# Kernel optimization log

Measured on AMD Instinct MI355X. Metric: run time of the kernel, lower is better.

## Reference

```python
import jax, jax.numpy as jnp
import numpy as np

B = 32
C = 768
NH = 12
HD = C // NH
P = 16
IMG = 224
G = IMG // P           # 14 patches per side
NP = G * G             # 196 patches
DEPTH = 12
PRUNE = [1, 1, 1, 1, 0.5, 0.5, 0.5, 0.5, 0.5, 0.5, 0.5, 0.5]
MOM = 0.5              # momentum for global class-attention update
TRADE = 0.5            # slow-fast tradeoff for placeholder token update
SCALE = HD ** -0.5
NCLS = 1000

def _ln(x, g, b, eps=1e-6):
    mu = jnp.mean(x, -1, keepdims=True)
    var = jnp.mean((x - mu) ** 2, -1, keepdims=True)
    return (x - mu) * jax.lax.rsqrt(var + eps) * g + b

def setup_inputs():
    key = jax.random.key(0)
    ks = iter(jax.random.split(key, 40))
    def rn(shape, s=0.02):
        return jax.random.normal(next(ks), shape, jnp.float32) * s
    return {
        'x_img': jax.random.normal(next(ks), (B, 3, IMG, IMG), jnp.float32),
        'cls_token': rn((1, 1, C)),
        'pos_embed': rn((1, NP + 1, C)),
        'patch_w': rn((3 * P * P, C)),
        'patch_b': rn((C,)),
        'ln1_g': jnp.ones((DEPTH, C), jnp.float32),
        'ln1_b': jnp.zeros((DEPTH, C), jnp.float32),
        'qk_w': rn((DEPTH, C, 2 * C)),
        'qk_b': rn((DEPTH, 2 * C)),
        'v_w': rn((DEPTH, C, C)),
        'v_b': rn((DEPTH, C)),
        'proj_w': rn((DEPTH, C, C)),
        'proj_b': rn((DEPTH, C)),
        'ln2_g': jnp.ones((DEPTH, C), jnp.float32),
        'ln2_b': jnp.zeros((DEPTH, C), jnp.float32),
        'fc1_w': rn((DEPTH, C, 4 * C)),
        'fc1_b': rn((DEPTH, 4 * C)),
        'fc2_w': rn((DEPTH, 4 * C, C)),
        'fc2_b': rn((DEPTH, C)),
        'norm_g': jnp.ones((C,), jnp.float32),
        'norm_b': jnp.zeros((C,), jnp.float32),
        'head_w': rn((C, NCLS)),
        'head_b': rn((NCLS,)),
    }

def reference(x_img, cls_token, pos_embed, patch_w, patch_b, ln1_g, ln1_b,
              qk_w, qk_b, v_w, v_b, proj_w, proj_b, ln2_g, ln2_b,
              fc1_w, fc1_b, fc2_w, fc2_b, norm_g, norm_b, head_w, head_b):
    Bq = x_img.shape[0]
    # PatchEmbed: Conv2d(k=P, stride=P) == flatten each patch as (c, ph, pw) then matmul
    patches = x_img.reshape(Bq, 3, G, P, G, P).transpose(0, 2, 4, 1, 3, 5)
    patches = patches.reshape(Bq, NP, 3 * P * P)
    x = patches @ patch_w + patch_b                                   # [B,196,C]
    x = jnp.concatenate([jnp.broadcast_to(cls_token, (Bq, 1, C)), x], 1)
    x = x + pos_embed                                                 # [B,197,C]

    def block(xt, i):
        # QKAttention + VAttention + proj residual, then MlpBlock residual.
        t = _ln(xt, ln1_g[i], ln1_b[i])
        Nt = t.shape[1]
        qk = (t @ qk_w[i] + qk_b[i]).reshape(Bq, Nt, 2, NH, HD)
        q = qk[:, :, 0].transpose(0, 2, 1, 3)                         # [B,H,Nt,hd]
        k = qk[:, :, 1].transpose(0, 2, 1, 3)
        attn = jax.nn.softmax(jnp.einsum('bhnd,bhmd->bhnm', q, k) * SCALE, -1)
        v = (t @ v_w[i] + v_b[i]).reshape(Bq, Nt, NH, HD).transpose(0, 2, 1, 3)
        o = jnp.einsum('bhnm,bhmd->bhnd', attn, v).transpose(0, 2, 1, 3).reshape(Bq, Nt, C)
        xt = xt + (o @ proj_w[i] + proj_b[i])
        h = _ln(xt, ln2_g[i], ln2_b[i])
        xt = xt + (jax.nn.gelu(h @ fc1_w[i] + fc1_b[i], approximate=False) @ fc2_w[i] + fc2_b[i])
        row = attn[:, :, 0, 1:].sum(1)   # cls-attention row, summed over heads
        return xt, row

    cls_attn = None
    for i in range(DEPTH):
        if PRUNE[i] == 1:
            x, row = block(x, i)
            cls_attn = row if cls_attn is None else (1 - MOM) * cls_attn + MOM * row
        else:
            N_ = int(NP * PRUNE[i])                        # informative token count
            idx = jnp.argsort(-cls_attn, axis=1)           # sort patches by score (easy_gather)
            xp = jnp.take_along_axis(x[:, 1:], idx[:, :, None], axis=1)
            cls_attn = jnp.take_along_axis(cls_attn, idx, axis=1)
            fast = xp[:, N_:]                              # placeholder (pruned) tokens
            score = cls_attn[:, N_:]
            rep = (fast * score[:, :, None]).sum(1, keepdims=True) \
                  / score.sum(1, keepdims=True)[:, :, None]  # representative token
            xs = jnp.concatenate([x[:, :1], xp[:, :N_], rep], 1)   # [B,N_+2,C]
            xs, row = block(xs, i)
            cls_attn = jnp.concatenate(
                [(1 - MOM) * cls_attn[:, :N_] + MOM * row[:, :N_], cls_attn[:, N_:]], 1)
            fast = fast + TRADE * (xs[:, -1:] - rep)       # fast update via rep residual
            x = jnp.concatenate([xs[:, :N_ + 1], fast], 1)  # back to [B,197,C]

    x = _ln(x, norm_g, norm_b)
    return x[:, 0] @ head_w + head_b                        # [B,1000]
```

## Files before the change

### kernel.cpp

```cpp
#include <hip/hip_runtime.h>
#include <hip/hip_bf16.h>
#include <stdint.h>

#define B_ 32
#define C_ 768
#define NH_ 12
#define HD_ 64
#define NP_ 196
#define NTOK 197
#define NKEEP 98
#define NCLS_ 1000
#define MPAD 6400
#define RS_ (3 * C_)

typedef __bf16 bf16x8 __attribute__((ext_vector_type(8)));
typedef float f32x4 __attribute__((ext_vector_type(4)));

__device__ __forceinline__ float blockReduceSum256(float v) {
    __shared__ float red[4];
    const int lane = threadIdx.x & 63, w = threadIdx.x >> 6;
#pragma unroll
    for (int off = 32; off; off >>= 1) v += __shfl_down(v, off);
    __syncthreads();
    if (lane == 0) red[w] = v;
    __syncthreads();
    return red[0] + red[1] + red[2] + red[3];
}

__device__ __forceinline__ void gload16(void* lds, const void* g) {
    __builtin_amdgcn_global_load_lds(
        (const __attribute__((address_space(1))) void*)g,
        (__attribute__((address_space(3))) void*)lds,
        16, 0, 0);
}

__global__ __launch_bounds__(256) void patchify_kernel(const float* __restrict__ img,
                                                       __hip_bfloat16* __restrict__ patches)
{
    const int bp = blockIdx.x;
    const int b = bp / NP_, p = bp % NP_;
    const int gy = p / 14, gx = p % 14;
    const int tid = threadIdx.x;
#pragma unroll
    for (int j = 0; j < 3; ++j) {
        const int e = tid + j * 256;
        const int c = e >> 8, rem = e & 255, py = rem >> 4, px = rem & 15;
        patches[(size_t)bp * C_ + e] = __float2bfloat16(
            img[(((size_t)b * 3 + c) * 224 + gy * 16 + py) * 224 + gx * 16 + px]);
    }
}

__global__ __launch_bounds__(256) void assemble_x_kernel(const float* __restrict__ pemb,
                                                         const float* __restrict__ cls_tok,
                                                         const float* __restrict__ pos,
                                                         float* __restrict__ x)
{
    const int b = blockIdx.x, t = blockIdx.y, tid = threadIdx.x;
#pragma unroll
    for (int j = 0; j < 3; ++j) {
        const int c = tid + j * 256;
        const float v = (t == 0) ? cls_tok[c] : pemb[((size_t)b * NP_ + (t - 1)) * C_ + c];
        x[((size_t)b * NTOK + t) * C_ + c] = v + pos[(size_t)t * C_ + c];
    }
}

__global__ __launch_bounds__(256) void ln_kernel(const float* __restrict__ x,
                                                 const float* __restrict__ g,
                                                 const float* __restrict__ b,
                                                 __hip_bfloat16* outB, float* outF,
                                                 long long inRowStride, int nRows)
{
    const int row = (blockIdx.x << 2) + (threadIdx.x >> 6);
    const int lane = threadIdx.x & 63;
    if (row >= nRows) return;
    const float* xr = x + (size_t)row * inRowStride;
    float4 v0 = *(const float4*)(xr + (lane << 2));
    float4 v1 = *(const float4*)(xr + 256 + (lane << 2));
    float4 v2 = *(const float4*)(xr + 512 + (lane << 2));
    float s = v0.x + v0.y + v0.z + v0.w + v1.x + v1.y + v1.z + v1.w
            + v2.x + v2.y + v2.z + v2.w;
#pragma unroll
    for (int off = 1; off < 64; off <<= 1) s += __shfl_xor(s, off);
    const float mu = s * (1.f / C_);
    float q = 0.f;
    {
        float d;
        d = v0.x - mu; q += d * d; d = v0.y - mu; q += d * d;
        d = v0.z - mu; q += d * d; d = v0.w - mu; q += d * d;
        d = v1.x - mu; q += d * d; d = v1.y - mu; q += d * d;
        d = v1.z - mu; q += d * d; d = v1.w - mu; q += d * d;
        d = v2.x - mu; q += d * d; d = v2.y - mu; q += d * d;
        d = v2.z - mu; q += d * d; d = v2.w - mu; q += d * d;
    }
#pragma unroll
    for (int off = 1; off < 64; off <<= 1) q += __shfl_xor(q, off);
    const float rs = rsqrtf(q * (1.f / C_) + 1e-6f);
    const float4 vv[3] = {v0, v1, v2};
#pragma unroll
    for (int j = 0; j < 3; ++j) {
        const int cbase = (j << 8) + (lane << 2);
        const float4 gv = *(const float4*)(g + cbase);
        const float4 bv = *(const float4*)(b + cbase);
        float o0 = (vv[j].x - mu) * rs * gv.x + bv.x;
        float o1 = (vv[j].y - mu) * rs * gv.y + bv.y;
        float o2 = (vv[j].z - mu) * rs * gv.z + bv.z;
        float o3 = (vv[j].w - mu) * rs * gv.w + bv.w;
        if (outB) {
            union { unsigned short us[4]; uint2 u; } pk;
            __hip_bfloat16 h;
            h = __float2bfloat16(o0); pk.us[0] = *(unsigned short*)&h;
            h = __float2bfloat16(o1); pk.us[1] = *(unsigned short*)&h;
            h = __float2bfloat16(o2); pk.us[2] = *(unsigned short*)&h;
            h = __float2bfloat16(o3); pk.us[3] = *(unsigned short*)&h;
            *(uint2*)((unsigned short*)outB + (size_t)row * C_ + cbase) = pk.u;
        }
        if (outF) {
            float4 o; o.x = o0; o.y = o1; o.z = o2; o.w = o3;
            *(float4*)(outF + (size_t)row * C_ + cbase) = o;
        }
    }
}

__global__ __launch_bounds__(256) void transpose_bf16_kernel(const float* __restrict__ W,
                                                             __hip_bfloat16* __restrict__ Wt,
                                                             int K, int N,
                                                             long long outLstride, long long outOff)
{
    __shared__ float tile[32][33];
    const size_t loffIn = (size_t)blockIdx.z * K * N;
    const size_t loffOut = (size_t)blockIdx.z * outLstride + outOff;
    const int k0 = blockIdx.y << 5, n0 = blockIdx.x << 5;
    const int tid = threadIdx.x;
#pragma unroll
    for (int e = tid; e < 1024; e += 256) {
        const int r = e >> 5, c = e & 31;
        tile[r][c] = W[loffIn + (size_t)(k0 + r) * N + n0 + c];
    }
    __syncthreads();
#pragma unroll
    for (int e = tid; e < 1024; e += 256) {
        const int r = e >> 5, c = e & 31;
        Wt[loffOut + (size_t)(n0 + r) * K + k0 + c] = __float2bfloat16(tile[c][r]);
    }
}

__global__ __launch_bounds__(256) void concat_bias_kernel(const float* __restrict__ qk_b,
                                                          const float* __restrict__ v_b,
                                                          float* __restrict__ out)
{
    const int i = blockIdx.x * 256 + threadIdx.x;
    if (i < 12 * RS_) {
        const int l = i / RS_, c = i % RS_;
        out[i] = (c < 2 * C_) ? qk_b[l * 2 * C_ + c] : v_b[l * C_ + (c - 2 * C_)];
    }
}

template<int GELU, int OMODE>
__global__ __launch_bounds__(256) void gemm_bf16_kernel(const __hip_bfloat16* __restrict__ A,
                                                        const __hip_bfloat16* __restrict__ Bt,
                                                        const float* __restrict__ bias,
                                                        const float* __restrict__ res,
                                                        float* __restrict__ outF,
                                                        __hip_bfloat16* __restrict__ outB,
                                                        int K, int N)
{
    __shared__ __align__(16) unsigned short sAB[2][128 * 64];
    unsigned short* sA = sAB[0];
    unsigned short* sB = sAB[1];
    const int tid = threadIdx.x;
    const int wv = tid >> 6, ln = tid & 63;

    const int nwg = gridDim.x * gridDim.y;
    int lid = blockIdx.y * gridDim.x + blockIdx.x;
    {
        const int q = nwg >> 3, r = nwg & 7;
        const int xcd = lid & 7, lq = lid >> 3;
        lid = (xcd < r ? xcd * (q + 1) : r * (q + 1) + (xcd - r) * q) + lq;
    }
    const int bn = (lid % gridDim.x) << 7;
    const int bm = (lid / gridDim.x) << 7;

    const int wr = wv >> 1, wc = wv & 1;
    const int ln15 = ln & 15, lhi = ln >> 4;

    const int srow = tid >> 3;
    const int gc = (tid & 7) ^ ((tid >> 3) & 7);
    const __hip_bfloat16* gA = A + (size_t)(bm + srow) * K + (gc << 3);
    const __hip_bfloat16* gB = Bt + (size_t)(bn + srow) * K + (gc << 3);
    unsigned short* lA = sA + (wv << 9);
    unsigned short* lB = sB + (wv << 9);

    f32x4 acc[4][4] = {};
    const int swk = ln15 & 7;
    for (int k0 = 0; k0 < K; k0 += 64) {
#pragma unroll
        for (int i = 0; i < 4; ++i) {
            gload16(lA + (i << 11), gA + (size_t)(i << 5) * K + k0);
            gload16(lB + (i << 11), gB + (size_t)(i << 5) * K + k0);
        }
        __syncthreads();
#pragma unroll
        for (int kk = 0; kk < 2; ++kk) {
            const int ch = ((kk << 2) + lhi) ^ swk;
            bf16x8 a[4], b[4];
#pragma unroll
            for (int m = 0; m < 4; ++m)
                a[m] = *(const bf16x8*)(sA + (((wr << 6) + (m << 4) + ln15) << 6) + (ch << 3));
#pragma unroll
            for (int n = 0; n < 4; ++n)
                b[n] = *(const bf16x8*)(sB + (((wc << 6) + (n << 4) + ln15) << 6) + (ch << 3));
#pragma unroll
            for (int m = 0; m < 4; ++m)
#pragma unroll
                for (int n = 0; n < 4; ++n)
                    acc[m][n] = __builtin_amdgcn_mfma_f32_16x16x32_bf16(a[m], b[n], acc[m][n], 0, 0, 0);
        }
        __syncthreads();
    }

    if (OMODE == 0) {
        unsigned short* sOut = sAB[0];
#pragma unroll
        for (int n = 0; n < 4; ++n) {
            const int col = (wc << 6) + (n << 4) + ln15;
            const float bv = bias[bn + col];
#pragma unroll
            for (int m = 0; m < 4; ++m) {
                const int row0 = (wr << 6) + (m << 4) + (lhi << 2);
#pragma unroll
                for (int r = 0; r < 4; ++r) {
                    float x = acc[m][n][r] + bv;
                    if (GELU) x = 0.5f * x * (1.f + erff(x * 0.70710678118654752f));
                    const __hip_bfloat16 hb = __float2bfloat16(x);
                    sOut[(row0 + r) * 128 + col] = *(const unsigned short*)&hb;
                }
            }
        }
        __syncthreads();
#pragma unroll
        for (int i = 0; i < 8; ++i) {
            const int chunk = (i << 8) + tid;
            const int row = chunk >> 4, c8 = (chunk & 15) << 3;
            *(uint4*)((unsigned short*)outB + (size_t)(bm + row) * N + bn + c8) =
                *(const uint4*)(sOut + row * 128 + c8);
        }
    } else {
#pragma unroll
        for (int n = 0; n < 4; ++n) {
            const int gcn = bn + (wc << 6) + (n << 4) + ln15;
            const float bv = bias[gcn];
#pragma unroll
            for (int m = 0; m < 4; ++m) {
                const int gr0 = bm + (wr << 6) + (m << 4) + (lhi << 2);
                f32x4 v = acc[m][n];
#pragma unroll
                for (int r = 0; r < 4; ++r) {
                    const size_t o = (size_t)(gr0 + r) * N + gcn;
                    float x = v[r] + bv;
                    if (OMODE == 1) x += res[o];
                    outF[o] = x;
                }
            }
        }
    }
}

__global__ __launch_bounds__(256) void head_kernel(const float* __restrict__ A,
                                                   const float* __restrict__ W,
                                                   const float* __restrict__ bias,
                                                   float* __restrict__ out)
{
    const int n = blockIdx.x * 256 + threadIdx.x;
    const int m = blockIdx.y;
    if (n >= NCLS_) return;
    const float* a = A + (size_t)m * C_;
    float s = 0.f;
#pragma unroll 8
    for (int k = 0; k < C_; ++k) s = fmaf(a[k], W[(size_t)k * NCLS_ + n], s);
    out[(size_t)m * NCLS_ + n] = s + bias[n];
}

template<int NT16>
__global__ __launch_bounds__(256) void attn_mfma_kernel(const __hip_bfloat16* __restrict__ qkv,
                                                        __hip_bfloat16* __restrict__ o,
                                                        float* __restrict__ attn0,
                                                        int Nt)
{
    constexpr int NPAD = NT16 * 16;
    constexpr int PSW = (((NPAD / 8) & 7) == 0) ? 7 : 3;
    constexpr int VSW = 7;
    constexpr int PROWB = NPAD * 2 + 16;
    constexpr int VROWB = (NPAD == 224) ? 528 : 272;
    __shared__ unsigned short sK[NPAD * 64 + 512];
    __shared__ unsigned short sV[32 * VROWB];

    const int bh = blockIdx.x;
    const int b = bh / NH_, h = bh % NH_;
    const int qtile = blockIdx.y;
    const int tid = threadIdx.x, ln = tid & 63, wv = tid >> 6;
    const int ln15 = ln & 15, lhi = ln >> 4;
    const __hip_bfloat16* qkbase = qkv + (size_t)b * Nt * RS_;

#pragma unroll
    for (int it = 0; it < NPAD * 8 / 256; ++it) {
        const int p = it * 256 + tid;
        int key = p >> 3;
        const int c = (p & 7) ^ (key & 7);
        if (key >= Nt) key = Nt - 1;
        unsigned short* dst = sK + (size_t)(it * 256 + (wv << 6)) * 8;
        gload16(dst, qkbase + (size_t)key * RS_ + C_ + (h << 6) + (c << 3));
    }
#pragma unroll
    for (int it = 0; it < NPAD * 8 / 256; ++it) {
        const int e = it * 256 + tid;
        const int key = e >> 3, dc = e & 7;
        union { uint4 u; unsigned short us[8]; } val;
        val.u = make_uint4(0u, 0u, 0u, 0u);
        if (key < Nt)
            val.u = *(const uint4*)(qkbase + (size_t)key * RS_ + 2 * C_ + (h << 6) + (dc << 3));
        const int kc = key >> 3, kb = (key & 7) << 1;
#pragma unroll
        for (int j = 0; j < 8; ++j) {
            const int d = (dc << 3) + j;
            *(unsigned short*)((char*)sV + d * VROWB + ((kc ^ ((d >> 3) & VSW)) << 4) + kb) = val.us[j];
        }
    }
    const int qbase = qtile * 64 + (wv << 4);
    int qrow = qbase + ln15; if (qrow >= Nt) qrow = Nt - 1;
    const __hip_bfloat16* qp = qkbase + (size_t)qrow * RS_ + (h << 6) + (lhi << 3);
    const bf16x8 qf0 = *(const bf16x8*)qp;
    const bf16x8 qf1 = *(const bf16x8*)(qp + 32);
    __syncthreads();

    f32x4 sc[NT16];
#pragma unroll
    for (int t = 0; t < NT16; ++t) {
        const int key = (t << 4) + ln15;
        const unsigned short* kr = sK + (size_t)key * 64;
        const bf16x8 k0 = *(const bf16x8*)(kr + ((lhi ^ (key & 7)) << 3));
        const bf16x8 k1 = *(const bf16x8*)(kr + (((4 + lhi) ^ (key & 7)) << 3));
        f32x4 a = {0.f, 0.f, 0.f, 0.f};
        a = __builtin_amdgcn_mfma_f32_16x16x32_bf16(k0, qf0, a, 0, 0, 0);
        a = __builtin_amdgcn_mfma_f32_16x16x32_bf16(k1, qf1, a, 0, 0, 0);
        sc[t] = a;
    }
    __syncthreads();

    float mx = -1e30f;
#pragma unroll
    for (int t = 0; t < NT16; ++t)
#pragma unroll
        for (int r = 0; r < 4; ++r) {
            const int key = (t << 4) + (lhi << 2) + r;
            const float v = (key < Nt) ? sc[t][r] * 0.125f : -1e30f;
            sc[t][r] = v;
            mx = fmaxf(mx, v);
        }
    mx = fmaxf(mx, __shfl_xor(mx, 16));
    mx = fmaxf(mx, __shfl_xor(mx, 32));
    float sum = 0.f;
#pragma unroll
    for (int t = 0; t < NT16; ++t)
#pragma unroll
        for (int r = 0; r < 4; ++r) {
            const float e = expf(sc[t][r] - mx);
            sc[t][r] = e; sum += e;
        }
    sum += __shfl_xor(sum, 16);
    sum += __shfl_xor(sum, 32);
    const float inv = 1.f / sum;

    char* Pw = (char*)sK + wv * (16 * PROWB);
    const bool isQ0 = (qtile == 0) && (wv == 0) && (ln15 == 0);
#pragma unroll
    for (int t = 0; t < NT16; ++t) {
        union { unsigned short us[4]; uint2 u2; } pk;
#pragma unroll
        for (int r = 0; r < 4; ++r) {
            const float p = sc[t][r] * inv;
            const __hip_bfloat16 hb = __float2bfloat16(p);
            pk.us[r] = *(const unsigned short*)&hb;
            if (isQ0) {
                const int key = (t << 4) + (lhi << 2) + r;
                if (key < Nt) attn0[(size_t)bh * NTOK + key] = p;
            }
        }
        const int chunk = ((t << 1) + (lhi >> 1)) ^ (ln15 & PSW);
        *(uint2*)(Pw + ln15 * PROWB + (chunk << 4) + ((lhi & 1) << 3)) = pk.u2;
    }
    __syncthreads();

    f32x4 oa[4] = {};
#pragma unroll
    for (int s = 0; s < NPAD / 32; ++s) {
        const bf16x8 pf = *(const bf16x8*)(Pw + ln15 * PROWB +
                                           ((((s << 2) + lhi) ^ (ln15 & PSW)) << 4));
#pragma unroll
        for (int n = 0; n < 4; ++n) {
            const int d = (n << 4) + ln15;
            const bf16x8 vf = *(const bf16x8*)((char*)sV + d * VROWB +
                                               ((((s << 2) + lhi) ^ ((d >> 3) & VSW)) << 4));
            oa[n] = __builtin_amdgcn_mfma_f32_16x16x32_bf16(pf, vf, oa[n], 0, 0, 0);
        }
    }
#pragma unroll
    for (int n = 0; n < 4; ++n)
#pragma unroll
        for (int r = 0; r < 4; ++r) {
            const int qq = qbase + (lhi << 2) + r;
            if (qq < Nt)
                o[((size_t)b * Nt + qq) * C_ + (h << 6) + (n << 4) + ln15] =
                    __float2bfloat16(oa[n][r]);
        }
}

__global__ __launch_bounds__(256) void row_cls_ema_kernel(const float* __restrict__ attn0,
                                                          float* __restrict__ cls, int first)
{
    const int b = blockIdx.x, t = threadIdx.x;
    if (t < NP_) {
        float s = 0.f;
#pragma unroll
        for (int h = 0; h < NH_; ++h) s += attn0[((size_t)(b * NH_ + h)) * NTOK + 1 + t];
        const int i = b * NP_ + t;
        cls[i] = first ? s : 0.5f * cls[i] + 0.5f * s;
    }
}

__global__ __launch_bounds__(256) void row_cls_prune_kernel(const float* __restrict__ attn0,
                                                            const float* __restrict__ sorted,
                                                            float* __restrict__ cls)
{
    const int b = blockIdx.x, t = threadIdx.x;
    if (t < NP_) {
        float sv = sorted[b * NP_ + t];
        if (t < NKEEP) {
            float s = 0.f;
#pragma unroll
            for (int h = 0; h < NH_; ++h) s += attn0[((size_t)(b * NH_ + h)) * NTOK + 1 + t];
            sv = 0.5f * sv + 0.5f * s;
        }
        cls[b * NP_ + t] = sv;
    }
}

__global__ __launch_bounds__(256) void rank_kernel(const float* __restrict__ cls,
                                                   int* __restrict__ idx,
                                                   float* __restrict__ sorted,
                                                   float* __restrict__ ssum)
{
    __shared__ float sv[NP_];
    const int b = blockIdx.x, t = threadIdx.x;
    if (t < NP_) sv[t] = cls[b * NP_ + t];
    __syncthreads();
    float val = 0.f; int r = NP_;
    if (t < NP_) {
        val = sv[t];
        r = 0;
        for (int j = 0; j < NP_; ++j) {
            const float vj = sv[j];
            r += (vj > val || (vj == val && j < t)) ? 1 : 0;
        }
        idx[b * NP_ + r] = t;
        sorted[b * NP_ + r] = val;
    }
    const float contrib = (t < NP_ && r >= NKEEP) ? val : 0.f;
    const float tot = blockReduceSum256(contrib);
    if (t == 0) ssum[b] = tot;
}

__global__ __launch_bounds__(256) void build_xs_kernel(const float* __restrict__ x,
                                                       const int* __restrict__ idx,
                                                       const float* __restrict__ sorted,
                                                       const float* __restrict__ ssum,
                                                       float* __restrict__ xs,
                                                       float* __restrict__ fast,
                                                       float* __restrict__ rep)
{
    const int b = blockIdx.x, t = blockIdx.y, tid = threadIdx.x;
    const float* xb = x + (size_t)b * NTOK * C_;
    if (t == 0) {
#pragma unroll
        for (int j = 0; j < 3; ++j) {
            const int c = tid + j * 256;
            xs[(size_t)b * 100 * C_ + c] = xb[c];
        }
    } else if (t <= NKEEP) {
        const int src = 1 + idx[b * NP_ + (t - 1)];
#pragma unroll
        for (int j = 0; j < 3; ++j) {
            const int c = tid + j * 256;
            xs[((size_t)b * 100 + t) * C_ + c] = xb[(size_t)src * C_ + c];
        }
    } else if (t == NKEEP + 1) {
        const float inv = 1.f / ssum[b];
        float acc0 = 0.f, acc1 = 0.f, acc2 = 0.f;
        for (int jj = 0; jj < NP_ - NKEEP; ++jj) {
            const int src = 1 + idx[b * NP_ + NKEEP + jj];
            const float wgt = sorted[b * NP_ + NKEEP + jj];
            const float* xr = xb + (size_t)src * C_;
            acc0 = fmaf(xr[tid], wgt, acc0);
            acc1 = fmaf(xr[tid + 256], wgt, acc1);
            acc2 = fmaf(xr[tid + 512], wgt, acc2);
        }
        float* xsr = xs + ((size_t)b * 100 + 99) * C_;
        float* rr = rep + (size_t)b * C_;
        xsr[tid] = acc0 * inv;       rr[tid] = acc0 * inv;
        xsr[tid + 256] = acc1 * inv; rr[tid + 256] = acc1 * inv;
        xsr[tid + 512] = acc2 * inv; rr[tid + 512] = acc2 * inv;
    } else {
        const int jf = t - (NKEEP + 2);
        const int src = 1 + idx[b * NP_ + NKEEP + jf];
#pragma unroll
        for (int j = 0; j < 3; ++j) {
            const int c = tid + j * 256;
            fast[((size_t)b * (NP_ - NKEEP) + jf) * C_ + c] = xb[(size_t)src * C_ + c];
        }
    }
}

__global__ __launch_bounds__(256) void scatter_back_kernel(const float* __restrict__ xs,
                                                           const float* __restrict__ fast,
                                                           const float* __restrict__ rep,
                                                           float* __restrict__ x)
{
    const int b = blockIdx.x, t = blockIdx.y, tid = threadIdx.x;
#pragma unroll
    for (int j = 0; j < 3; ++j) {
        const int c = tid + j * 256;
        float v;
        if (t <= NKEEP)
            v = xs[((size_t)b * 100 + t) * C_ + c];
        else
            v = fast[((size_t)b * (NP_ - NKEEP) + (t - NKEEP - 1)) * C_ + c]
                + 0.5f * (xs[((size_t)b * 100 + 99) * C_ + c] - rep[(size_t)b * C_ + c]);
        x[((size_t)b * NTOK + t) * C_ + c] = v;
    }
}

extern "C" void kernel_launch(void* const* d_in, const int* in_sizes, int n_in,
                              void* d_out, int out_size, void* d_ws, size_t ws_size,
                              hipStream_t stream)
{
    (void)in_sizes; (void)n_in; (void)out_size;
    const float* x_img   = (const float*)d_in[0];
    const float* cls_tok = (const float*)d_in[1];
    const float* pos     = (const float*)d_in[2];
    const float* patch_w = (const float*)d_in[3];
    const float* patch_b = (const float*)d_in[4];
    const float* ln1_g   = (const float*)d_in[5];
    const float* ln1_b   = (const float*)d_in[6];
    const float* qk_w    = (const float*)d_in[7];
    const float* qk_b    = (const float*)d_in[8];
    const float* v_w     = (const float*)d_in[9];
    const float* v_b     = (const float*)d_in[10];
    const float* proj_w  = (const float*)d_in[11];
    const float* proj_b  = (const float*)d_in[12];
    const float* ln2_g   = (const float*)d_in[13];
    const float* ln2_b   = (const float*)d_in[14];
    const float* fc1_w   = (const float*)d_in[15];
    const float* fc1_b   = (const float*)d_in[16];
    const float* fc2_w   = (const float*)d_in[17];
    const float* fc2_b   = (const float*)d_in[18];
    const float* norm_g  = (const float*)d_in[19];
    const float* norm_b  = (const float*)d_in[20];
    const float* head_w  = (const float*)d_in[21];
    const float* head_b  = (const float*)d_in[22];

    char* base = (char*)d_ws;
    size_t off = 0;
    auto alloc = [&](size_t bytes) -> void* {
        void* p = base + off; off = (off + bytes + 255) & ~(size_t)255; return p;
    };
    float* X    = (float*)alloc((size_t)MPAD * C_ * 4);
    __hip_bfloat16* Tb   = (__hip_bfloat16*)alloc((size_t)MPAD * C_ * 2);
    __hip_bfloat16* QKVb = (__hip_bfloat16*)alloc((size_t)MPAD * RS_ * 2);
    __hip_bfloat16* Hb   = (__hip_bfloat16*)alloc((size_t)MPAD * 4 * C_ * 2);
    float* XS   = (float*)alloc((size_t)3200 * C_ * 4);
    float* FAST = (float*)alloc((size_t)B_ * (NP_ - NKEEP) * C_ * 4);
    float* REP  = (float*)alloc((size_t)B_ * C_ * 4);
    float* ATTN0= (float*)alloc((size_t)B_ * NH_ * NTOK * 4);
    float* CLS  = (float*)alloc((size_t)B_ * NP_ * 4);
    float* SORT = (float*)alloc((size_t)B_ * NP_ * 4);
    float* SSUM = (float*)alloc((size_t)B_ * 4);
    float* T0   = (float*)alloc((size_t)B_ * C_ * 4);
    int*   IDX  = (int*)alloc((size_t)B_ * NP_ * 4);
    float* BIASQKV = (float*)alloc((size_t)12 * RS_ * 4);
    __hip_bfloat16* WTpatch = (__hip_bfloat16*)alloc((size_t)C_ * C_ * 2);
    __hip_bfloat16* WTqkv   = (__hip_bfloat16*)alloc((size_t)12 * RS_ * C_ * 2);
    __hip_bfloat16* WTproj  = (__hip_bfloat16*)alloc((size_t)12 * C_ * C_ * 2);
    __hip_bfloat16* WTfc1   = (__hip_bfloat16*)alloc((size_t)12 * C_ * 4 * C_ * 2);
    __hip_bfloat16* WTfc2   = (__hip_bfloat16*)alloc((size_t)12 * 4 * C_ * C_ * 2);
    if (off > ws_size) return;

    __hip_bfloat16* Ob    = Hb;
    __hip_bfloat16* PATCH = Hb;
    float*          PEMB  = (float*)QKVb;

    const dim3 blk(256);

    transpose_bf16_kernel<<<dim3(24, 24, 1), blk, 0, stream>>>(patch_w, WTpatch, C_, C_, (long long)C_ * C_, 0);
    transpose_bf16_kernel<<<dim3(48, 24, 12), blk, 0, stream>>>(qk_w, WTqkv, C_, 2 * C_, (long long)RS_ * C_, 0);
    transpose_bf16_kernel<<<dim3(24, 24, 12), blk, 0, stream>>>(v_w, WTqkv, C_, C_, (long long)RS_ * C_, (long long)2 * C_ * C_);
    transpose_bf16_kernel<<<dim3(24, 24, 12), blk, 0, stream>>>(proj_w, WTproj, C_, C_, (long long)C_ * C_, 0);
    transpose_bf16_kernel<<<dim3(96, 24, 12), blk, 0, stream>>>(fc1_w, WTfc1, C_, 4 * C_, (long long)4 * C_ * C_, 0);
    transpose_bf16_kernel<<<dim3(24, 96, 12), blk, 0, stream>>>(fc2_w, WTfc2, 4 * C_, C_, (long long)4 * C_ * C_, 0);
    concat_bias_kernel<<<(12 * RS_ + 255) / 256, blk, 0, stream>>>(qk_b, v_b, BIASQKV);

    auto runBlock = [&](int i, float* xb, int Nt) {
        const int M = B_ * Nt;
        const int mt = (M + 127) >> 7;
        const int qtiles = (Nt + 63) >> 6;
        ln_kernel<<<(M + 3) / 4, blk, 0, stream>>>(xb, ln1_g + i * C_, ln1_b + i * C_, Tb, nullptr, C_, M);
        gemm_bf16_kernel<0, 0><<<dim3(RS_ / 128, mt), blk, 0, stream>>>(
            Tb, WTqkv + (size_t)i * RS_ * C_, BIASQKV + (size_t)i * RS_, nullptr, nullptr, QKVb, C_, RS_);
        if (Nt == NTOK)
            attn_mfma_kernel<14><<<dim3(B_ * NH_, qtiles), blk, 0, stream>>>(QKVb, Ob, ATTN0, Nt);
        else
            attn_mfma_kernel<8><<<dim3(B_ * NH_, qtiles), blk, 0, stream>>>(QKVb, Ob, ATTN0, Nt);
        gemm_bf16_kernel<0, 1><<<dim3(6, mt), blk, 0, stream>>>(
            Ob, WTproj + (size_t)i * C_ * C_, proj_b + (size_t)i * C_, xb, xb, nullptr, C_, C_);
        ln_kernel<<<(M + 3) / 4, blk, 0, stream>>>(xb, ln2_g + i * C_, ln2_b + i * C_, Tb, nullptr, C_, M);
        gemm_bf16_kernel<1, 0><<<dim3(24, mt), blk, 0, stream>>>(
            Tb, WTfc1 + (size_t)i * C_ * 4 * C_, fc1_b + (size_t)i * 4 * C_, nullptr, nullptr, Hb, C_, 4 * C_);
        gemm_bf16_kernel<0, 1><<<dim3(6, mt), blk, 0, stream>>>(
            Hb, WTfc2 + (size_t)i * 4 * C_ * C_, fc2_b + (size_t)i * C_, xb, xb, nullptr, 4 * C_, C_);
    };

    patchify_kernel<<<B_ * NP_, blk, 0, stream>>>(x_img, PATCH);
    gemm_bf16_kernel<0, 2><<<dim3(6, 49), blk, 0, stream>>>(
        PATCH, WTpatch, patch_b, nullptr, PEMB, nullptr, C_, C_);
    assemble_x_kernel<<<dim3(B_, NTOK), blk, 0, stream>>>(PEMB, cls_tok, pos, X);

    for (int i = 0; i < 12; ++i) {
        if (i < 4) {
            runBlock(i, X, NTOK);
            row_cls_ema_kernel<<<B_, blk, 0, stream>>>(ATTN0, CLS, i == 0 ? 1 : 0);
        } else {
            rank_kernel<<<B_, blk, 0, stream>>>(CLS, IDX, SORT, SSUM);
            build_xs_kernel<<<dim3(B_, 198), blk, 0, stream>>>(X, IDX, SORT, SSUM, XS, FAST, REP);
            runBlock(i, XS, 100);
            scatter_back_kernel<<<dim3(B_, NTOK), blk, 0, stream>>>(XS, FAST, REP, X);
            row_cls_prune_kernel<<<B_, blk, 0, stream>>>(ATTN0, SORT, CLS);
        }
    }

    ln_kernel<<<8, blk, 0, stream>>>(X, norm_g, norm_b, nullptr, T0, (long long)NTOK * C_, B_);
    head_kernel<<<dim3(4, B_), blk, 0, stream>>>(T0, head_w, head_b, (float*)d_out);
}
```

Measured before the change: 2.797 ms.

## Double-buffer LDS in bf16 GEMM to overlap global loads with MFMA

Doubles the GEMM's shared-memory footprint to two A/B buffer pairs. The next K tile is loaded directly into LDS while MFMAs run on the current one, using explicit vmcnt waits and raw barriers. LDS reads become inline ds_read_b128 with precomputed row offsets and a sched barrier. This hides global-load latency behind compute, at the cost of 64KB LDS per block, which can lower occupancy. It also relies on the assumption that the K tile count is even or handled by the tail.

```diff
diff --git a/kernel.cpp b/kernel.cpp
--- a/kernel.cpp
+++ b/kernel.cpp
@@ -164,9 +164,7 @@
                                                         __hip_bfloat16* __restrict__ outB,
                                                         int K, int N)
 {
-    __shared__ __align__(16) unsigned short sAB[2][128 * 64];
-    unsigned short* sA = sAB[0];
-    unsigned short* sB = sAB[1];
+    __shared__ __align__(16) unsigned short sLDS[4][128 * 64];
     const int tid = threadIdx.x;
     const int wv = tid >> 6, ln = tid & 63;
 
@@ -187,39 +185,77 @@
     const int gc = (tid & 7) ^ ((tid >> 3) & 7);
     const __hip_bfloat16* gA = A + (size_t)(bm + srow) * K + (gc << 3);
     const __hip_bfloat16* gB = Bt + (size_t)(bn + srow) * K + (gc << 3);
-    unsigned short* lA = sA + (wv << 9);
-    unsigned short* lB = sB + (wv << 9);
+
+    const unsigned ldsBase =
+        (unsigned)(size_t)(__attribute__((address_space(3))) unsigned short*)&sLDS[0][0];
+    unsigned rowA[4], rowB[4];
+#pragma unroll
+    for (int m = 0; m < 4; ++m) rowA[m] = (unsigned)(((wr << 6) + (m << 4) + ln15) << 7);
+#pragma unroll
+    for (int n = 0; n < 4; ++n) rowB[n] = (unsigned)(((wc << 6) + (n << 4) + ln15) << 7);
+    const int swk = ln15 & 7;
 
     f32x4 acc[4][4] = {};
-    const int swk = ln15 & 7;
-    for (int k0 = 0; k0 < K; k0 += 64) {
+
+    auto stage = [&](int bufA, int bufB, int k0) {
 #pragma unroll
         for (int i = 0; i < 4; ++i) {
-            gload16(lA + (i << 11), gA + (size_t)(i << 5) * K + k0);
-            gload16(lB + (i << 11), gB + (size_t)(i << 5) * K + k0);
-        }
-        __syncthreads();
+            gload16(&sLDS[bufA][(wv << 9) + (i << 11)], gA + (size_t)(i << 5) * K + k0);
+            gload16(&sLDS[bufB][(wv << 9) + (i << 11)], gB + (size_t)(i << 5) * K + k0);
+        }
+    };
+    auto compute = [&](unsigned aOff, unsigned bOff) {
 #pragma unroll
         for (int kk = 0; kk < 2; ++kk) {
-            const int ch = ((kk << 2) + lhi) ^ swk;
+            const unsigned chb = (unsigned)(((((kk << 2) + lhi)) ^ swk) << 4);
             bf16x8 a[4], b[4];
 #pragma unroll
             for (int m = 0; m < 4; ++m)
-                a[m] = *(const bf16x8*)(sA + (((wr << 6) + (m << 4) + ln15) << 6) + (ch << 3));
+                asm volatile("ds_read_b128 %0, %1"
+                             : "=v"(a[m]) : "v"(ldsBase + aOff + rowA[m] + chb));
 #pragma unroll
             for (int n = 0; n < 4; ++n)
-                b[n] = *(const bf16x8*)(sB + (((wc << 6) + (n << 4) + ln15) << 6) + (ch << 3));
+                asm volatile("ds_read_b128 %0, %1"
+                             : "=v"(b[n]) : "v"(ldsBase + bOff + rowB[n] + chb));
+            asm volatile("s_waitcnt lgkmcnt(0)" ::: "memory");
+            __builtin_amdgcn_sched_barrier(0);
 #pragma unroll
             for (int m = 0; m < 4; ++m)
 #pragma unroll
                 for (int n = 0; n < 4; ++n)
                     acc[m][n] = __builtin_amdgcn_mfma_f32_16x16x32_bf16(a[m], b[n], acc[m][n], 0, 0, 0);
         }
-        __syncthreads();
-    }
+    };
+
+    const int ntiles = K >> 6;
+    stage(0, 1, 0);
+    asm volatile("s_waitcnt vmcnt(0)" ::: "memory");
+    __builtin_amdgcn_s_barrier();
+    int t = 0;
+    for (; t + 2 < ntiles; t += 2) {
+        stage(2, 3, (t + 1) << 6);
+        asm volatile("s_waitcnt vmcnt(8)" ::: "memory");
+        __builtin_amdgcn_s_barrier();
+        compute(0u, 16384u);
+        __builtin_amdgcn_s_barrier();
+        stage(0, 1, (t + 2) << 6);
+        asm volatile("s_waitcnt vmcnt(8)" ::: "memory");
+        __builtin_amdgcn_s_barrier();
+        compute(32768u, 49152u);
+        __builtin_amdgcn_s_barrier();
+    }
+    stage(2, 3, (ntiles - 1) << 6);
+    asm volatile("s_waitcnt vmcnt(8)" ::: "memory");
+    __builtin_amdgcn_s_barrier();
+    compute(0u, 16384u);
+    __builtin_amdgcn_s_barrier();
+    asm volatile("s_waitcnt vmcnt(0)" ::: "memory");
+    __builtin_amdgcn_s_barrier();
+    compute(32768u, 49152u);
+    __syncthreads();
 
     if (OMODE == 0) {
-        unsigned short* sOut = sAB[0];
+        unsigned short* sOut = &sLDS[0][0];
 #pragma unroll
         for (int n = 0; n < 4; ++n) {
             const int col = (wc << 6) + (n << 4) + ln15;
```

After: 2.727 ms. 2.5% less time.
